# Kernel tuning notes

Hardware: AMD Instinct MI355X
Metric: run time of the kernel (lower is better)

The kernel has to match this reference:

```python
import jax, jax.numpy as jnp
import numpy as np
import math

INPUT_DIM = 1024
EMBED_DIM = 1024
NUM_HEADS = 16
HEAD_DIM = EMBED_DIM // NUM_HEADS


def setup_inputs() -> dict:
    key = jax.random.key(0)
    k_x, k_qkv, k_out_w, k_out_b = jax.random.split(key, 4)
    x = jax.random.normal(k_x, (1, 4096, INPUT_DIM), dtype=jnp.float32)
    # nn.Linear weights are [out, in]; kaiming-uniform-ish scale
    s1 = 1.0 / math.sqrt(INPUT_DIM)
    s2 = 1.0 / math.sqrt(EMBED_DIM)
    qkv_w = jax.random.uniform(k_qkv, (3 * EMBED_DIM, INPUT_DIM), jnp.float32, -s1, s1)
    out_w = jax.random.uniform(k_out_w, (EMBED_DIM, EMBED_DIM), jnp.float32, -s2, s2)
    out_b = jax.random.uniform(k_out_b, (EMBED_DIM,), jnp.float32, -s2, s2)
    return {"x": x, "qkv_w": qkv_w, "out_w": out_w, "out_b": out_b}


def reference(x, qkv_w, out_w, out_b):
    B, N, C = x.shape
    qkv = jnp.einsum('bnc,ec->bne', x, qkv_w)  # [B,N,3E]
    q = qkv[:, :, 0:EMBED_DIM].reshape(B, N, NUM_HEADS, HEAD_DIM)
    k = qkv[:, :, EMBED_DIM:2 * EMBED_DIM].reshape(B, N, NUM_HEADS, HEAD_DIM)
    v = qkv[:, :, 2 * EMBED_DIM:].reshape(B, N, NUM_HEADS, HEAD_DIM)
    scores = jnp.einsum('bihd,bjhd->bhij', q, k) / jnp.sqrt(jnp.float32(HEAD_DIM))
    attn = jax.nn.softmax(scores, axis=-1)  # [B,H,N,N]
    out = jnp.einsum('bhik,bkhd->bhid', attn, v)
    out = out.transpose(0, 2, 1, 3).reshape(B, N, EMBED_DIM)
    return jnp.einsum('bne,fe->bnf', out, out_w) + out_b
```

## Files before the change

### kernel.cpp

```cpp
#include <hip/hip_runtime.h>
#include <hip/hip_bf16.h>

typedef __bf16 bf16;
typedef bf16 bf16x8 __attribute__((ext_vector_type(8)));
typedef bf16 bf16x4 __attribute__((ext_vector_type(4)));
typedef float f32x4 __attribute__((ext_vector_type(4)));

#define MFMA16(a, b, c) __builtin_amdgcn_mfma_f32_16x16x32_bf16(a, b, c, 0, 0, 0)

__device__ __forceinline__ void g2l16(const bf16* g, bf16* l) {
  __builtin_amdgcn_global_load_lds(
      (__attribute__((address_space(1))) void*)(void*)g,
      (__attribute__((address_space(3))) void*)l,
      16, 0, 0);
}

__global__ void sniff_dtype(const void* __restrict__ x, int* __restrict__ flag) {
  const unsigned short* u = (const unsigned short*)x;
  const int lane = threadIdx.x;
  unsigned short v = u[lane];
  int e = (v >> 7) & 0xFF;
  int sane = (e == 0) || (e >= 112 && e <= 142);
  unsigned long long m = __ballot(sane);
  if (lane == 0) flag[0] = (__popcll(m) >= 56) ? 1 : 0;
}

__global__ void convert_to_bf16(const void* __restrict__ in, bf16* __restrict__ out,
                                long n8, const int* __restrict__ flag) {
  long i = (long)blockIdx.x * 256 + threadIdx.x;
  if (i >= n8) return;
  if (*flag) {
    ((bf16x8*)out)[i] = ((const bf16x8*)in)[i];
  } else {
    const float4* p = (const float4*)in;
    float4 a = p[i * 2], b = p[i * 2 + 1];
    bf16x8 v;
    v[0] = (bf16)a.x; v[1] = (bf16)a.y; v[2] = (bf16)a.z; v[3] = (bf16)a.w;
    v[4] = (bf16)b.x; v[5] = (bf16)b.y; v[6] = (bf16)b.z; v[7] = (bf16)b.w;
    ((bf16x8*)out)[i] = v;
  }
}

__global__ __launch_bounds__(256) void gemm_qkv(
    const bf16* __restrict__ A, const bf16* __restrict__ B,
    bf16* __restrict__ qB, bf16* __restrict__ kP, bf16* __restrict__ vP) {
  __shared__ __align__(16) bf16 As[128 * 32];
  __shared__ __align__(16) bf16 Bs[128 * 32];

  const int tid  = threadIdx.x;
  const int lane = tid & 63;
  const int wave = tid >> 6;
  const int wm   = wave >> 1, wn = wave & 1;
  const int l15  = lane & 15, quad = lane >> 4;
  const long m0 = (long)blockIdx.x * 128;
  const long n0 = (long)blockIdx.y * 128;
  const int  K  = 1024;

  const bf16* Ab = A + m0 * K;
  const bf16* Bb = B + n0 * K;
  const int rowA = tid & 127;
  const int dc   = tid >> 7;

  f32x4 acc[4][4] = {};

  for (int k0 = 0; k0 < K; k0 += 32) {
    g2l16(Ab + (long)rowA * K + k0 + dc * 8,       As + tid * 8);
    g2l16(Ab + (long)rowA * K + k0 + (dc + 2) * 8, As + (tid + 256) * 8);
    g2l16(Bb + (long)rowA * K + k0 + dc * 8,       Bs + tid * 8);
    g2l16(Bb + (long)rowA * K + k0 + (dc + 2) * 8, Bs + (tid + 256) * 8);
    __syncthreads();

    bf16x8 af[4], bfr[4];
#pragma unroll
    for (int t = 0; t < 4; t++) {
      af[t]  = *(const bf16x8*)(As + (quad * 128 + wm * 64 + t * 16 + l15) * 8);
      bfr[t] = *(const bf16x8*)(Bs + (quad * 128 + wn * 64 + t * 16 + l15) * 8);
    }
#pragma unroll
    for (int tm = 0; tm < 4; tm++)
#pragma unroll
      for (int tn = 0; tn < 4; tn++)
        acc[tm][tn] = MFMA16(af[tm], bfr[tn], acc[tm][tn]);
    __syncthreads();
  }

  const long rb = m0 + wm * 64;
  const long cb = n0 + wn * 64;
  const int third = (int)(n0 >> 10);
  const float QSC = 0.125f * 1.44269504088896f;

#pragma unroll
  for (int tm = 0; tm < 4; tm++) {
#pragma unroll
    for (int tn = 0; tn < 4; tn++) {
      const long r0 = rb + tm * 16 + quad * 4;
      const long c  = cb + tn * 16 + l15;
      if (third == 0) {
#pragma unroll
        for (int r = 0; r < 4; r++)
          qB[(r0 + r) * 1024 + c] = (bf16)(acc[tm][tn][r] * QSC);
      } else if (third == 1) {
        const int ep = (int)c - 1024;
        const int h = ep >> 6, d = ep & 63;
        const long bhd = (long)h * 64 * 4096 + (long)((d >> 3) * 64) * 8 + (d & 7);
#pragma unroll
        for (int r = 0; r < 4; r++) {
          const int n = (int)(r0 + r);
          const int kt = n >> 6, kpos = n & 63;
          const int tn_ = 2 * (kpos >> 5) + ((kpos >> 2) & 1);
          const int m   = tn_ * 16 + ((kpos >> 3) & 3) * 4 + (kpos & 3);
          kP[bhd + (long)kt * 4096 + m * 8] = (bf16)acc[tm][tn][r];
        }
      } else {
        const int ep = (int)c - 2048;
        const int h = ep >> 6, d = ep & 63;
#pragma unroll
        for (int r = 0; r < 4; r++) {
          const int n = (int)(r0 + r);
          const int kt = n >> 6, pc = (n & 63) >> 3, j = n & 7;
          vP[(long)(h * 64 + kt) * 4096 + (pc * 64 + d) * 8 + j] = (bf16)acc[tm][tn][r];
        }
      }
    }
  }
}

template <bool BIAS, bool DYNOUT>
__global__ __launch_bounds__(256) void gemm_bt(
    const bf16* __restrict__ A, const bf16* __restrict__ B,
    void* __restrict__ Cv, const bf16* __restrict__ bias,
    int M, int Nn, int K, const int* __restrict__ oflag) {
  __shared__ __align__(16) bf16 As[128 * 32];
  __shared__ __align__(16) bf16 Bs[128 * 32];

  const int tid  = threadIdx.x;
  const int lane = tid & 63;
  const int wave = tid >> 6;
  const int wm   = wave >> 1, wn = wave & 1;
  const int l15  = lane & 15, quad = lane >> 4;
  const long m0 = (long)blockIdx.x * 128;
  const long n0 = (long)blockIdx.y * 128;

  const bf16* Ab = A + m0 * K;
  const bf16* Bb = B + n0 * K;
  const int rowA = tid & 127;
  const int dc   = tid >> 7;

  f32x4 acc[4][4] = {};

  for (int k0 = 0; k0 < K; k0 += 32) {
    g2l16(Ab + (long)rowA * K + k0 + dc * 8,       As + tid * 8);
    g2l16(Ab + (long)rowA * K + k0 + (dc + 2) * 8, As + (tid + 256) * 8);
    g2l16(Bb + (long)rowA * K + k0 + dc * 8,       Bs + tid * 8);
    g2l16(Bb + (long)rowA * K + k0 + (dc + 2) * 8, Bs + (tid + 256) * 8);
    __syncthreads();

    bf16x8 af[4], bfr[4];
#pragma unroll
    for (int t = 0; t < 4; t++) {
      af[t]  = *(const bf16x8*)(As + (quad * 128 + wm * 64 + t * 16 + l15) * 8);
      bfr[t] = *(const bf16x8*)(Bs + (quad * 128 + wn * 64 + t * 16 + l15) * 8);
    }
#pragma unroll
    for (int tm = 0; tm < 4; tm++)
#pragma unroll
      for (int tn = 0; tn < 4; tn++)
        acc[tm][tn] = MFMA16(af[tm], bfr[tn], acc[tm][tn]);
    __syncthreads();
  }

  const int obf = DYNOUT ? *oflag : 1;
  const long rb = m0 + wm * 64;
  const long cb = n0 + wn * 64;
#pragma unroll
  for (int tm = 0; tm < 4; tm++) {
#pragma unroll
    for (int tn = 0; tn < 4; tn++) {
      const long r0 = rb + tm * 16 + quad * 4;
      const long c  = cb + tn * 16 + l15;
      const float bv = BIAS ? (float)bias[c] : 0.0f;
#pragma unroll
      for (int r = 0; r < 4; r++) {
        const float val = acc[tm][tn][r] + bv;
        const long idx = (r0 + r) * Nn + c;
        if (DYNOUT && !obf) ((float*)Cv)[idx] = val;
        else                ((bf16*)Cv)[idx]  = (bf16)val;
      }
    }
  }
}

__global__ __launch_bounds__(128) void flash_attn(
    const bf16* __restrict__ qB, const bf16* __restrict__ kP,
    const bf16* __restrict__ vP, bf16* __restrict__ O) {
  __shared__ __align__(16) bf16 Ks[64 * 64];
  __shared__ __align__(16) bf16 Vs[64 * 64];

  const int tid = threadIdx.x;
  const int lane = tid & 63;
  const int wq = tid >> 6;
  const int l15 = lane & 15, quad = lane >> 4;
  const int qt = blockIdx.x, h = blockIdx.y;
  const int q0 = qt * 64;

  bf16x8 qf[2][2];
#pragma unroll
  for (int g = 0; g < 2; g++) {
    const bf16* qrow = qB + (long)(q0 + wq * 32 + g * 16 + l15) * 1024 + h * 64;
    qf[g][0] = *(const bf16x8*)(qrow + quad * 8);
    qf[g][1] = *(const bf16x8*)(qrow + 32 + quad * 8);
  }

  f32x4 oa[2][4] = {};
  float l_sum[2] = {0.0f, 0.0f};

  const bf16* kb = kP + (long)h * 64 * 4096;
  const bf16* vb = vP + (long)h * 64 * 4096;

  for (int kt = 0; kt < 64; kt++) {
    const bf16* kbase = kb + (long)kt * 4096;
    const bf16* vbase = vb + (long)kt * 4096;
    __syncthreads();
#pragma unroll
    for (int i = 0; i < 4; i++) {
      g2l16(kbase + (tid + i * 128) * 8, Ks + (tid + i * 128) * 8);
      g2l16(vbase + (tid + i * 128) * 8, Vs + (tid + i * 128) * 8);
    }
    __syncthreads();

    f32x4 s[2][4];
#pragma unroll
    for (int tn = 0; tn < 4; tn++) {
      bf16x8 a0 = *(const bf16x8*)(Ks + ((quad)*64 + tn * 16 + l15) * 8);
      bf16x8 a1 = *(const bf16x8*)(Ks + ((4 + quad) * 64 + tn * 16 + l15) * 8);
      f32x4 z0 = {}; z0 = MFMA16(a0, qf[0][0], z0); z0 = MFMA16(a1, qf[0][1], z0);
      f32x4 z1 = {}; z1 = MFMA16(a0, qf[1][0], z1); z1 = MFMA16(a1, qf[1][1], z1);
      s[0][tn] = z0; s[1][tn] = z1;
    }

    bf16x8 pf[2][2];
#pragma unroll
    for (int g = 0; g < 2; g++)
#pragma unroll
      for (int tn = 0; tn < 4; tn++)
#pragma unroll
        for (int r = 0; r < 4; r++) {
          float p = __builtin_amdgcn_exp2f(s[g][tn][r]);
          l_sum[g] += p;
          pf[g][tn >> 1][(tn & 1) * 4 + r] = (bf16)p;
        }

#pragma unroll
    for (int tm = 0; tm < 4; tm++) {
      bf16x8 v0 = *(const bf16x8*)(Vs + ((quad)*64 + tm * 16 + l15) * 8);
      bf16x8 v1 = *(const bf16x8*)(Vs + ((4 + quad) * 64 + tm * 16 + l15) * 8);
      oa[0][tm] = MFMA16(v0, pf[0][0], oa[0][tm]);
      oa[0][tm] = MFMA16(v1, pf[0][1], oa[0][tm]);
      oa[1][tm] = MFMA16(v0, pf[1][0], oa[1][tm]);
      oa[1][tm] = MFMA16(v1, pf[1][1], oa[1][tm]);
    }
  }

#pragma unroll
  for (int g = 0; g < 2; g++) {
    float l = l_sum[g];
    l += __shfl_xor(l, 16, 64);
    l += __shfl_xor(l, 32, 64);
    const float inv = 1.0f / l;
    bf16* orow = O + (long)(q0 + wq * 32 + g * 16 + l15) * 1024 + h * 64;
#pragma unroll
    for (int tm = 0; tm < 4; tm++) {
      bf16x4 v;
#pragma unroll
      for (int r = 0; r < 4; r++) v[r] = (bf16)(oa[g][tm][r] * inv);
      *(bf16x4*)(orow + tm * 16 + quad * 4) = v;
    }
  }
}

extern "C" void kernel_launch(void* const* d_in, const int* in_sizes, int n_in,
                              void* d_out, int out_size, void* d_ws, size_t ws_size,
                              hipStream_t stream) {
  const void* x     = d_in[0];
  const void* qkv_w = d_in[1];
  const void* out_w = d_in[2];
  const void* out_b = d_in[3];

  char* ws = (char*)d_ws;
  int*  flag = (int*)ws;
  bf16* qB   = (bf16*)(ws + 4096);
  bf16* kP   = (bf16*)(ws + 4096 + 8388608);
  bf16* vP   = (bf16*)(ws + 4096 + 16777216);
  bf16* ob   = (bf16*)(ws + 4096 + 25165824);
  bf16* qwb  = (bf16*)(ws + 4096 + 33554432);
  bf16* xb   = ob;
  bf16* owb  = qB;
  bf16* obb  = qB + 1048576;

  sniff_dtype<<<1, 64, 0, stream>>>(x, flag);
  convert_to_bf16<<<2048, 256, 0, stream>>>(x, xb, 524288, flag);
  convert_to_bf16<<<1536, 256, 0, stream>>>(qkv_w, qwb, 393216, flag);

  gemm_qkv<<<dim3(32, 24), 256, 0, stream>>>(xb, qwb, qB, kP, vP);

  flash_attn<<<dim3(64, 16), 128, 0, stream>>>(qB, kP, vP, ob);

  convert_to_bf16<<<512, 256, 0, stream>>>(out_w, owb, 131072, flag);
  convert_to_bf16<<<1, 256, 0, stream>>>(out_b, obb, 128, flag);

  gemm_bt<true, true><<<dim3(32, 8), 256, 0, stream>>>(
      ob, owb, d_out, obb, 4096, 1024, 1024, flag);
}
```

Baseline: 266.9 us.

## Double-buffer K/V tiles in flash attention and widen blocks to four waves

The attention kernel now uses two LDS buffers for K and V. It prefetches the next key tile with async global-to-LDS loads while computing on the current one, which removes the second barrier per iteration. Blocks grow from two to four waves covering 128 queries, so each loaded K/V tile serves twice as many queries and the grid halves. In exchange, LDS use doubles and block count drops, which may lower occupancy. Correctness relies on the barrier waiting for the outstanding async loads.

```diff
diff --git a/kernel.cpp b/kernel.cpp
--- a/kernel.cpp
+++ b/kernel.cpp
@@ -190,23 +190,23 @@
   }
 }
 
-__global__ __launch_bounds__(128) void flash_attn(
+__global__ __launch_bounds__(256) void flash_attn(
     const bf16* __restrict__ qB, const bf16* __restrict__ kP,
     const bf16* __restrict__ vP, bf16* __restrict__ O) {
-  __shared__ __align__(16) bf16 Ks[64 * 64];
-  __shared__ __align__(16) bf16 Vs[64 * 64];
+  __shared__ __align__(16) bf16 Ks[2][64 * 64];
+  __shared__ __align__(16) bf16 Vs[2][64 * 64];
 
   const int tid = threadIdx.x;
   const int lane = tid & 63;
-  const int wq = tid >> 6;
+  const int wave = tid >> 6;
   const int l15 = lane & 15, quad = lane >> 4;
   const int qt = blockIdx.x, h = blockIdx.y;
-  const int q0 = qt * 64;
+  const int q0 = qt * 128;
 
   bf16x8 qf[2][2];
 #pragma unroll
   for (int g = 0; g < 2; g++) {
-    const bf16* qrow = qB + (long)(q0 + wq * 32 + g * 16 + l15) * 1024 + h * 64;
+    const bf16* qrow = qB + (long)(q0 + wave * 32 + g * 16 + l15) * 1024 + h * 64;
     qf[g][0] = *(const bf16x8*)(qrow + quad * 8);
     qf[g][1] = *(const bf16x8*)(qrow + 32 + quad * 8);
   }
@@ -217,22 +217,30 @@
   const bf16* kb = kP + (long)h * 64 * 4096;
   const bf16* vb = vP + (long)h * 64 * 4096;
 
+#pragma unroll
+  for (int i = 0; i < 2; i++) {
+    g2l16(kb + (tid + i * 256) * 8, Ks[0] + (tid + i * 256) * 8);
+    g2l16(vb + (tid + i * 256) * 8, Vs[0] + (tid + i * 256) * 8);
+  }
+
   for (int kt = 0; kt < 64; kt++) {
-    const bf16* kbase = kb + (long)kt * 4096;
-    const bf16* vbase = vb + (long)kt * 4096;
-    __syncthreads();
-#pragma unroll
-    for (int i = 0; i < 4; i++) {
-      g2l16(kbase + (tid + i * 128) * 8, Ks + (tid + i * 128) * 8);
-      g2l16(vbase + (tid + i * 128) * 8, Vs + (tid + i * 128) * 8);
-    }
-    __syncthreads();
+    const int cur = kt & 1;
+    __syncthreads();
+    if (kt + 1 < 64) {
+      const bf16* kbase = kb + (long)(kt + 1) * 4096;
+      const bf16* vbase = vb + (long)(kt + 1) * 4096;
+#pragma unroll
+      for (int i = 0; i < 2; i++) {
+        g2l16(kbase + (tid + i * 256) * 8, Ks[cur ^ 1] + (tid + i * 256) * 8);
+        g2l16(vbase + (tid + i * 256) * 8, Vs[cur ^ 1] + (tid + i * 256) * 8);
+      }
+    }
 
     f32x4 s[2][4];
 #pragma unroll
     for (int tn = 0; tn < 4; tn++) {
-      bf16x8 a0 = *(const bf16x8*)(Ks + ((quad)*64 + tn * 16 + l15) * 8);
-      bf16x8 a1 = *(const bf16x8*)(Ks + ((4 + quad) * 64 + tn * 16 + l15) * 8);
+      bf16x8 a0 = *(const bf16x8*)(Ks[cur] + ((quad)*64 + tn * 16 + l15) * 8);
+      bf16x8 a1 = *(const bf16x8*)(Ks[cur] + ((4 + quad) * 64 + tn * 16 + l15) * 8);
       f32x4 z0 = {}; z0 = MFMA16(a0, qf[0][0], z0); z0 = MFMA16(a1, qf[0][1], z0);
       f32x4 z1 = {}; z1 = MFMA16(a0, qf[1][0], z1); z1 = MFMA16(a1, qf[1][1], z1);
       s[0][tn] = z0; s[1][tn] = z1;
@@ -252,8 +260,8 @@
 
 #pragma unroll
     for (int tm = 0; tm < 4; tm++) {
-      bf16x8 v0 = *(const bf16x8*)(Vs + ((quad)*64 + tm * 16 + l15) * 8);
-      bf16x8 v1 = *(const bf16x8*)(Vs + ((4 + quad) * 64 + tm * 16 + l15) * 8);
+      bf16x8 v0 = *(const bf16x8*)(Vs[cur] + ((quad)*64 + tm * 16 + l15) * 8);
+      bf16x8 v1 = *(const bf16x8*)(Vs[cur] + ((4 + quad) * 64 + tm * 16 + l15) * 8);
       oa[0][tm] = MFMA16(v0, pf[0][0], oa[0][tm]);
       oa[0][tm] = MFMA16(v1, pf[0][1], oa[0][tm]);
       oa[1][tm] = MFMA16(v0, pf[1][0], oa[1][tm]);
@@ -267,7 +275,7 @@
     l += __shfl_xor(l, 16, 64);
     l += __shfl_xor(l, 32, 64);
     const float inv = 1.0f / l;
-    bf16* orow = O + (long)(q0 + wq * 32 + g * 16 + l15) * 1024 + h * 64;
+    bf16* orow = O + (long)(q0 + wave * 32 + g * 16 + l15) * 1024 + h * 64;
 #pragma unroll
     for (int tm = 0; tm < 4; tm++) {
       bf16x4 v;
@@ -303,7 +311,7 @@
 
   gemm_qkv<<<dim3(32, 24), 256, 0, stream>>>(xb, qwb, qB, kP, vP);
 
-  flash_attn<<<dim3(64, 16), 128, 0, stream>>>(qB, kP, vP, ob);
+  flash_attn<<<dim3(32, 16), 256, 0, stream>>>(qB, kP, vP, ob);
 
   convert_to_bf16<<<512, 256, 0, stream>>>(out_w, owb, 131072, flag);
   convert_to_bf16<<<1, 256, 0, stream>>>(out_b, obb, 128, flag);
```

After: 266.7 us. About the same (-0.1%).
